# Optimization experiments

Hardware: AMD Instinct MI355X
Metric: run time of the kernel (lower is better)

Reference implementation:

```python
import jax, jax.numpy as jnp
import numpy as np

N, E, D_IN, D_H, D_OUT = 100000, 1600000, 128, 128, 16


def setup_inputs() -> dict:
    key = jax.random.key(0)
    k_x, k_e, k_w1, k_w2 = jax.random.split(key, 4)
    x = jax.random.normal(k_x, (N, D_IN), dtype=jnp.float32)
    edge_index = jax.random.randint(k_e, (2, E), 0, N, dtype=jnp.int64)
    # glorot-ish init for the two GCNConv weight matrices
    W1 = jax.random.normal(k_w1, (D_IN, D_H), dtype=jnp.float32) * (1.0 / np.sqrt(D_IN))
    b1 = jnp.zeros((D_H,), dtype=jnp.float32)
    W2 = jax.random.normal(k_w2, (D_H, D_OUT), dtype=jnp.float32) * (1.0 / np.sqrt(D_H))
    b2 = jnp.zeros((D_OUT,), dtype=jnp.float32)
    return {"x": x, "edge_index": edge_index, "W1": W1, "b1": b1, "W2": W2, "b2": b2}


def _gcn_conv(x, src, dst, norm, W, b, n):
    # linear transform, gather from source nodes, normalize, scatter-add to targets
    h = x @ W                                   # [N, d_out]
    msg = h[src] * norm[:, None]                # [E+N, d_out]
    return jax.ops.segment_sum(msg, dst, num_segments=n) + b


def reference(x, edge_index, W1, b1, W2, b2):
    n = x.shape[0]
    # GCNConv default: add self-loops, symmetric normalization D^-1/2 A D^-1/2
    loops = jnp.arange(n, dtype=edge_index.dtype)
    src = jnp.concatenate([edge_index[0], loops])
    dst = jnp.concatenate([edge_index[1], loops])
    deg = jax.ops.segment_sum(jnp.ones_like(dst, dtype=x.dtype), dst, num_segments=n)
    dinv = jnp.where(deg > 0, jax.lax.rsqrt(deg), 0.0)
    norm = dinv[src] * dinv[dst]                # [E+N]

    h = _gcn_conv(x, src, dst, norm, W1, b1, n)
    h = jax.nn.relu(h)
    # dropout is identity in eval mode (reference uses eval / deterministic path)
    out = _gcn_conv(h, src, dst, norm, W2, b2, n)
    return out
```

## Files before the change

kernel.cpp:

```cpp
#include <hip/hip_runtime.h>

typedef unsigned int uint;
typedef __attribute__((ext_vector_type(8))) short bf16x8;
typedef __attribute__((ext_vector_type(4))) float f32x4;

#define D_IN 128
#define D_H  128
#define D_OUT 16
#define NPC 512
#define NPCSH 9
#define CLDS 224
#define P1 256
#define XL_STRIDE 68
#define WT_STRIDE 68

static __device__ __forceinline__ float bflo(uint u) { return __uint_as_float(u << 16); }
static __device__ __forceinline__ float bfhi(uint u) { return __uint_as_float(u & 0xFFFF0000u); }
static __device__ __forceinline__ uint f2bf(float f) {
    uint b = __float_as_uint(f);
    return (b + 0x7FFFu + ((b >> 16) & 1u)) >> 16;
}
static __device__ __forceinline__ uint pk(float a, float b) {
    return f2bf(a) | (f2bf(b) << 16);
}


__global__ __launch_bounds__(256) void k_p1hist(const int* __restrict__ dst, int E, int N, int C,
                                                int chunk, int* __restrict__ hist1) {
    __shared__ int h[CLDS];
    int t = threadIdx.x, b = blockIdx.x;
    for (int i = t; i < C; i += 256) h[i] = 0;
    __syncthreads();
    int e0 = b * chunk, e1 = min(e0 + chunk, E);
    for (int e = e0 + t; e < e1; e += 256) {
        int d = dst[e];
        d = max(0, min(d, N - 1));
        atomicAdd(&h[d >> NPCSH], 1);
    }
    __syncthreads();
    int* hg = hist1 + (size_t)b * C;
    for (int i = t; i < C; i += 256) hg[i] = h[i];
}

__global__ __launch_bounds__(1024) void k_p1scan(int* __restrict__ hist1, int C,
                                                 int* __restrict__ cbase) {
    __shared__ int col[CLDS];
    __shared__ int sdata[1024];
    int t = threadIdx.x;
    for (int i = t; i < C; i += 1024) {
        int sum = 0;
        for (int b = 0; b < P1; b++) sum += hist1[(size_t)b * C + i];
        col[i] = sum;
    }
    __syncthreads();
    int v = (t < C) ? col[t] : 0;
    sdata[t] = v;
    __syncthreads();
    for (int off = 1; off < 1024; off <<= 1) {
        int x = (t >= off) ? sdata[t - off] : 0;
        __syncthreads();
        sdata[t] += x;
        __syncthreads();
    }
    int pos = sdata[t] - v;
    if (t < C) cbase[t] = pos;
    if (t == 1023) cbase[C] = sdata[1023];
    if (t < C) {
        int run = pos;
        for (int b = 0; b < P1; b++) {
            size_t idx = (size_t)b * C + t;
            int c = hist1[idx];
            hist1[idx] = run;
            run += c;
        }
    }
}

__global__ __launch_bounds__(256) void k_p1fill(const int* __restrict__ src,
                                                const int* __restrict__ dst, int E, int N, int C,
                                                int chunk, const int* __restrict__ hist1,
                                                uint* __restrict__ binned1) {
    __shared__ int cur[CLDS];
    int t = threadIdx.x, b = blockIdx.x;
    const int* hg = hist1 + (size_t)b * C;
    for (int i = t; i < C; i += 256) cur[i] = hg[i];
    __syncthreads();
    int e0 = b * chunk, e1 = min(e0 + chunk, E);
    for (int e = e0 + t; e < e1; e += 256) {
        int d = dst[e];
        d = max(0, min(d, N - 1));
        int s = src[e];
        s = max(0, min(s, N - 1));
        int p = atomicAdd(&cur[d >> NPCSH], 1);
        binned1[p] = ((uint)(d & (NPC - 1)) << 17) | (uint)s;
    }
}

__global__ __launch_bounds__(256) void k_p2(const uint* __restrict__ binned1,
                                            const int* __restrict__ cbase, int N,
                                            int* __restrict__ ssrc, int* __restrict__ rowptr,
                                            int* __restrict__ deg, float* __restrict__ dinv) {
    __shared__ int ncnt[NPC], nbase_[NPC];
    __shared__ int sdata[256];
    int c = blockIdx.x, t = threadIdx.x;
    int start = cbase[c], end = cbase[c + 1];
    for (int i = t; i < NPC; i += 256) ncnt[i] = 0;
    __syncthreads();
    for (int j = start + t; j < end; j += 256) atomicAdd(&ncnt[binned1[j] >> 17], 1);
    __syncthreads();
    int v0 = ncnt[2 * t], v1 = ncnt[2 * t + 1];
    int s = v0 + v1;
    sdata[t] = s;
    __syncthreads();
    for (int off = 1; off < 256; off <<= 1) {
        int xv = (t >= off) ? sdata[t - off] : 0;
        __syncthreads();
        sdata[t] += xv;
        __syncthreads();
    }
    int pre = sdata[t] - s;
    nbase_[2 * t] = start + pre;
    nbase_[2 * t + 1] = start + pre + v0;
    __syncthreads();
    for (int i = t; i < NPC; i += 256) {
        int node = c * NPC + i;
        if (node < N) {
            deg[node] = ncnt[i];
            rowptr[node] = nbase_[i];
            dinv[node] = rsqrtf((float)ncnt[i] + 1.0f);
        }
    }
    __syncthreads();
    for (int i = t; i < NPC; i += 256) ncnt[i] = nbase_[i];
    __syncthreads();
    for (int j = start + t; j < end; j += 256) {
        uint pe = binned1[j];
        int p = atomicAdd(&ncnt[pe >> 17], 1);
        ssrc[p] = (int)(pe & 0x1FFFFu);
    }
}


__global__ __launch_bounds__(256) void k_gemm1(const float* __restrict__ x,
                                               const float* __restrict__ W1,
                                               const float* __restrict__ dinv, int N,
                                               uint* __restrict__ hs_b) {
    __shared__ uint Wt[128 * WT_STRIDE];
    __shared__ uint xl[64 * XL_STRIDE];
    int t = threadIdx.x;
    int row0 = blockIdx.x * 64;
    for (int p = t; p < 64 * 128; p += 256) {
        int k2 = p >> 7, f = p & 127;
        float w0 = W1[(size_t)(2 * k2) * 128 + f];
        float w1 = W1[(size_t)(2 * k2 + 1) * 128 + f];
        Wt[f * WT_STRIDE + k2] = pk(w0, w1);
    }
    const float2* x2 = (const float2*)x;
    for (int p = t; p < 64 * 64; p += 256) {
        int r = p >> 6, c = p & 63;
        int gr = row0 + r;
        float2 v = (gr < N) ? x2[(size_t)gr * 64 + c] : make_float2(0.f, 0.f);
        xl[r * XL_STRIDE + c] = pk(v.x, v.y);
    }
    __syncthreads();
    int w = t >> 6, lane = t & 63;
    int q = lane >> 4, m = lane & 15;
    bf16x8 afr[4][4];
#pragma unroll
    for (int rt = 0; rt < 4; rt++)
#pragma unroll
        for (int kc = 0; kc < 4; kc++)
            afr[rt][kc] = *(const bf16x8*)&xl[(rt * 16 + m) * XL_STRIDE + kc * 16 + q * 4];
    f32x4 acc[2][4];
#pragma unroll
    for (int c = 0; c < 2; c++)
#pragma unroll
        for (int rt = 0; rt < 4; rt++) acc[c][rt] = (f32x4){0.f, 0.f, 0.f, 0.f};
#pragma unroll
    for (int c = 0; c < 2; c++) {
        int f = w * 32 + c * 16 + m;
#pragma unroll
        for (int kc = 0; kc < 4; kc++) {
            bf16x8 bfr = *(const bf16x8*)&Wt[f * WT_STRIDE + kc * 16 + q * 4];
#pragma unroll
            for (int rt = 0; rt < 4; rt++)
                acc[c][rt] =
                    __builtin_amdgcn_mfma_f32_16x16x32_bf16(afr[rt][kc], bfr, acc[c][rt], 0, 0, 0);
        }
    }
    __syncthreads();
    uint* outl = xl;
#pragma unroll
    for (int rt = 0; rt < 4; rt++) {
        int gb = row0 + rt * 16 + q * 4;
        float4 dv;
        if (gb + 3 < N) {
            dv = *(const float4*)&dinv[gb];
        } else {
            dv.x = (gb < N) ? dinv[gb] : 0.f;
            dv.y = (gb + 1 < N) ? dinv[gb + 1] : 0.f;
            dv.z = (gb + 2 < N) ? dinv[gb + 2] : 0.f;
            dv.w = (gb + 3 < N) ? dinv[gb + 3] : 0.f;
        }
        float dr[4] = {dv.x, dv.y, dv.z, dv.w};
#pragma unroll
        for (int c = 0; c < 2; c++) {
            f32x4 a = acc[c][rt];
#pragma unroll
            for (int r = 0; r < 4; r++) {
                float v = a[r] * dr[r];
                float vn = __shfl_xor(v, 1);
                if (!(lane & 1)) {
                    int row = rt * 16 + q * 4 + r;
                    int cp = (w * 32 + c * 16 + m) >> 1;
                    outl[row * 65 + cp] = pk(v, vn);
                }
            }
        }
    }
    __syncthreads();
    for (int p = t; p < 64 * 64; p += 256) {
        int r = p >> 6, cc = p & 63;
        int gr = row0 + r;
        if (gr < N) hs_b[(size_t)gr * 64 + cc] = outl[r * 65 + cc];
    }
}


__global__ __launch_bounds__(256) void k_agg1(const uint* __restrict__ hs_b,
                                              const int* __restrict__ rowptr,
                                              const int* __restrict__ deg,
                                              const int* __restrict__ ssrc,
                                              const float* __restrict__ dinv,
                                              const float2* __restrict__ b1, int N,
                                              uint* __restrict__ rh_b) {
    int w = threadIdx.x >> 6, lane = threadIdx.x & 63;
    int d = blockIdx.x * 4 + w;
    if (d >= N) return;
    int start = rowptr[d], cnt = deg[d];
    uint sv = hs_b[(size_t)d * 64 + lane];
    float a0 = bflo(sv), a1 = bfhi(sv);
    int base = 0;
    while (base < cnt) {
        int nb = min(cnt - base, 64);
        int idxv = (lane < nb) ? ssrc[start + base + lane] : 0;
        int j = 0;
        for (; j + 16 <= nb; j += 16) {
            uint u[16];
#pragma unroll
            for (int q = 0; q < 16; q++) {
                int i = __shfl(idxv, j + q);
                u[q] = hs_b[(size_t)i * 64 + lane];
            }
#pragma unroll
            for (int q = 0; q < 16; q++) {
                a0 += bflo(u[q]);
                a1 += bfhi(u[q]);
            }
        }
        for (; j + 4 <= nb; j += 4) {
            uint u[4];
#pragma unroll
            for (int q = 0; q < 4; q++) {
                int i = __shfl(idxv, j + q);
                u[q] = hs_b[(size_t)i * 64 + lane];
            }
#pragma unroll
            for (int q = 0; q < 4; q++) {
                a0 += bflo(u[q]);
                a1 += bfhi(u[q]);
            }
        }
        for (; j < nb; j++) {
            int i = __shfl(idxv, j);
            uint u = hs_b[(size_t)i * 64 + lane];
            a0 += bflo(u);
            a1 += bfhi(u);
        }
        base += nb;
    }
    float sc = dinv[d];
    float2 bb = b1[lane];
    rh_b[(size_t)d * 64 + lane] =
        pk(fmaxf(fmaf(a0, sc, bb.x), 0.f), fmaxf(fmaf(a1, sc, bb.y), 0.f));
}


__global__ __launch_bounds__(256) void k_gemm2(const uint* __restrict__ rh_b,
                                               const float* __restrict__ W2,
                                               const float* __restrict__ dinv, int N,
                                               uint* __restrict__ h2_b) {
    __shared__ float Wl[D_H * D_OUT];
    int t = threadIdx.x;
    for (int i = t; i < D_H * D_OUT; i += 256) Wl[i] = W2[i];
    __syncthreads();
    int r = blockIdx.x * 256 + t;
    if (r >= N) return;
    const uint* xrow = rh_b + (size_t)r * 64;
    float acc[16];
#pragma unroll
    for (int f = 0; f < 16; f++) acc[f] = 0.f;
    for (int c = 0; c < 16; c++) {
        uint4 xv = *(const uint4*)(xrow + c * 4);
        uint xs[4] = {xv.x, xv.y, xv.z, xv.w};
#pragma unroll
        for (int u = 0; u < 4; u++) {
            int k = c * 8 + u * 2;
            float x0 = bflo(xs[u]), x1 = bfhi(xs[u]);
            const float* w0 = &Wl[k * 16];
            const float* w1 = &Wl[(k + 1) * 16];
#pragma unroll
            for (int f = 0; f < 16; f++) acc[f] = fmaf(x0, w0[f], acc[f]);
#pragma unroll
            for (int f = 0; f < 16; f++) acc[f] = fmaf(x1, w1[f], acc[f]);
        }
    }
    float sc = dinv[r];
    uint o[8];
#pragma unroll
    for (int q = 0; q < 8; q++) o[q] = pk(acc[2 * q] * sc, acc[2 * q + 1] * sc);
    *(uint4*)&h2_b[(size_t)r * 8] = make_uint4(o[0], o[1], o[2], o[3]);
    *(uint4*)&h2_b[(size_t)r * 8 + 4] = make_uint4(o[4], o[5], o[6], o[7]);
}


__global__ __launch_bounds__(256) void k_agg2(const uint* __restrict__ h2_b,
                                              const int* __restrict__ rowptr,
                                              const int* __restrict__ deg,
                                              const int* __restrict__ ssrc,
                                              const float* __restrict__ dinv,
                                              const float* __restrict__ b2, int N,
                                              float2* __restrict__ out) {
    int w = threadIdx.x >> 6, lane = threadIdx.x & 63;
    int d = blockIdx.x * 4 + w;
    if (d >= N) return;
    int slot = lane >> 3, jp = lane & 7;
    int start = rowptr[d], cnt = deg[d];
    float a0 = 0.f, a1 = 0.f;
    if (slot == 0) {
        uint sv = h2_b[(size_t)d * 8 + jp];
        a0 = bflo(sv);
        a1 = bfhi(sv);
    }
    int base = 0;
    while (base < cnt) {
        int nb = min(cnt - base, 64);
        int idxv = (lane < nb) ? ssrc[start + base + lane] : 0;
        int ngroups = (nb + 7) >> 3;
        for (int g = 0; g < ngroups; g++) {
            int j = g * 8 + slot;
            int i = __shfl(idxv, j);
            if (j < nb) {
                uint hv = h2_b[(size_t)i * 8 + jp];
                a0 += bflo(hv);
                a1 += bfhi(hv);
            }
        }
        base += nb;
    }
    a0 += __shfl_xor(a0, 8);
    a1 += __shfl_xor(a1, 8);
    a0 += __shfl_xor(a0, 16);
    a1 += __shfl_xor(a1, 16);
    a0 += __shfl_xor(a0, 32);
    a1 += __shfl_xor(a1, 32);
    if (slot == 0) {
        float di = dinv[d];
        out[(size_t)d * 8 + jp] =
            make_float2(fmaf(a0, di, b2[2 * jp]), fmaf(a1, di, b2[2 * jp + 1]));
    }
}


extern "C" void kernel_launch(void* const* d_in, const int* in_sizes, int n_in,
                              void* d_out, int out_size, void* d_ws, size_t ws_size,
                              hipStream_t stream) {
    const float* x  = (const float*)d_in[0];
    const int*   ei = (const int*)d_in[1];
    const float* W1 = (const float*)d_in[2];
    const float* b1 = (const float*)d_in[3];
    const float* W2 = (const float*)d_in[4];
    const float* b2 = (const float*)d_in[5];
    int N = in_sizes[0] / D_IN;
    int E = in_sizes[1] / 2;
    const int* src = ei;
    const int* dst = ei + E;
    int C = (N + NPC - 1) / NPC;
    int chunk = (E + P1 - 1) / P1;

    char* ws = (char*)d_ws;
    size_t off = 0;
    auto alloc = [&](size_t bytes) -> char* {
        char* p = ws + off;
        off = (off + bytes + 255) & ~(size_t)255;
        return p;
    };
    int*   hist1   = (int*)alloc((size_t)P1 * C * 4);
    int*   cbase   = (int*)alloc((size_t)(C + 1) * 4);
    uint*  binned1 = (uint*)alloc((size_t)E * 4);
    int*   ssrc    = (int*)alloc((size_t)E * 4);
    int*   rowptr  = (int*)alloc((size_t)N * 4);
    int*   deg     = (int*)alloc((size_t)N * 4);
    float* dinv    = (float*)alloc((size_t)N * 4);
    uint*  hs_b    = (uint*)alloc((size_t)N * 64 * 4);
    uint*  rh_b    = (uint*)alloc((size_t)N * 64 * 4);
    uint*  h2_b    = hs_b;

    k_p1hist<<<P1, 256, 0, stream>>>(dst, E, N, C, chunk, hist1);
    k_p1scan<<<1, 1024, 0, stream>>>(hist1, C, cbase);
    k_p1fill<<<P1, 256, 0, stream>>>(src, dst, E, N, C, chunk, hist1, binned1);
    k_p2<<<C, 256, 0, stream>>>(binned1, cbase, N, ssrc, rowptr, deg, dinv);
    k_gemm1<<<(N + 63) / 64, 256, 0, stream>>>(x, W1, dinv, N, hs_b);
    k_agg1<<<(N + 3) / 4, 256, 0, stream>>>(hs_b, rowptr, deg, ssrc, dinv,
                                            (const float2*)b1, N, rh_b);
    k_gemm2<<<(N + 255) / 256, 256, 0, stream>>>(rh_b, W2, dinv, N, h2_b);
    k_agg2<<<(N + 3) / 4, 256, 0, stream>>>(h2_b, rowptr, deg, ssrc, dinv, b2, N,
                                            (float2*)d_out);
}
```

Measured before the change: 320.4 us.

## Transpose histogram layout for parallel scan; persistent gemm1 with prepacked W1

Stores the per-block bucket histogram transposed (bucket-major), so the single-block scan kernel can process each bucket with one wavefront doing a vectorized int4 load and shuffle prefix scan. This replaces the old serial 256-iteration per-thread loops. W1 is now packed to bf16 once by a new small kernel, and gemm1 becomes a persistent grid-stride kernel capped at 768 blocks. Each block loads the packed weights into LDS once and reuses them across many 64-row tiles, reading x with float4 loads. The cost is an extra launch, and the fill and hist kernels now do strided hist accesses.

```diff
diff --git a/kernel.cpp b/kernel.cpp
--- a/kernel.cpp
+++ b/kernel.cpp
@@ -38,8 +38,7 @@
         atomicAdd(&h[d >> NPCSH], 1);
     }
     __syncthreads();
-    int* hg = hist1 + (size_t)b * C;
-    for (int i = t; i < C; i += 256) hg[i] = h[i];
+    for (int i = t; i < C; i += 256) hist1[(size_t)i * P1 + b] = h[i];
 }
 
 __global__ __launch_bounds__(1024) void k_p1scan(int* __restrict__ hist1, int C,
@@ -47,10 +46,23 @@
     __shared__ int col[CLDS];
     __shared__ int sdata[1024];
     int t = threadIdx.x;
-    for (int i = t; i < C; i += 1024) {
-        int sum = 0;
-        for (int b = 0; b < P1; b++) sum += hist1[(size_t)b * C + i];
-        col[i] = sum;
+    int w = t >> 6, lane = t & 63;
+    for (int i = w; i < C; i += 16) {
+        int4 v = ((const int4*)hist1)[i * 64 + lane];
+        int s = v.x + v.y + v.z + v.w;
+        int inc = s;
+        for (int off = 1; off < 64; off <<= 1) {
+            int o = __shfl_up(inc, off);
+            if (lane >= off) inc += o;
+        }
+        int excl = inc - s;
+        int4 p;
+        p.x = excl;
+        p.y = excl + v.x;
+        p.z = excl + v.x + v.y;
+        p.w = excl + v.x + v.y + v.z;
+        ((int4*)hist1)[i * 64 + lane] = p;
+        if (lane == 63) col[i] = inc;
     }
     __syncthreads();
     int v = (t < C) ? col[t] : 0;
@@ -65,14 +77,13 @@
     int pos = sdata[t] - v;
     if (t < C) cbase[t] = pos;
     if (t == 1023) cbase[C] = sdata[1023];
-    if (t < C) {
-        int run = pos;
-        for (int b = 0; b < P1; b++) {
-            size_t idx = (size_t)b * C + t;
-            int c = hist1[idx];
-            hist1[idx] = run;
-            run += c;
-        }
+    if (t < C) col[t] = pos;
+    __syncthreads();
+    for (int i = w; i < C; i += 16) {
+        int base = col[i];
+        int4 p = ((int4*)hist1)[i * 64 + lane];
+        p.x += base; p.y += base; p.z += base; p.w += base;
+        ((int4*)hist1)[i * 64 + lane] = p;
     }
 }
 
@@ -82,8 +93,7 @@
                                                 uint* __restrict__ binned1) {
     __shared__ int cur[CLDS];
     int t = threadIdx.x, b = blockIdx.x;
-    const int* hg = hist1 + (size_t)b * C;
-    for (int i = t; i < C; i += 256) cur[i] = hg[i];
+    for (int i = t; i < C; i += 256) cur[i] = hist1[(size_t)i * P1 + b];
     __syncthreads();
     int e0 = b * chunk, e1 = min(e0 + chunk, E);
     for (int e = e0 + t; e < e1; e += 256) {
@@ -141,88 +151,100 @@
 }
 
 
-__global__ __launch_bounds__(256) void k_gemm1(const float* __restrict__ x,
-                                               const float* __restrict__ W1,
+__global__ __launch_bounds__(256) void k_packW1(const float* __restrict__ W1,
+                                                uint* __restrict__ W1p) {
+    int t = blockIdx.x * 256 + threadIdx.x;
+    if (t >= 64 * 128) return;
+    int k2 = t >> 7, f = t & 127;
+    float w0 = W1[(size_t)(2 * k2) * 128 + f];
+    float w1 = W1[(size_t)(2 * k2 + 1) * 128 + f];
+    W1p[t] = pk(w0, w1);
+}
+
+
+__global__ __launch_bounds__(256) void k_gemm1(const uint* __restrict__ W1p,
+                                               const float* __restrict__ x,
                                                const float* __restrict__ dinv, int N,
-                                               uint* __restrict__ hs_b) {
+                                               uint* __restrict__ hs_b, int ntiles) {
     __shared__ uint Wt[128 * WT_STRIDE];
     __shared__ uint xl[64 * XL_STRIDE];
     int t = threadIdx.x;
-    int row0 = blockIdx.x * 64;
     for (int p = t; p < 64 * 128; p += 256) {
         int k2 = p >> 7, f = p & 127;
-        float w0 = W1[(size_t)(2 * k2) * 128 + f];
-        float w1 = W1[(size_t)(2 * k2 + 1) * 128 + f];
-        Wt[f * WT_STRIDE + k2] = pk(w0, w1);
-    }
-    const float2* x2 = (const float2*)x;
-    for (int p = t; p < 64 * 64; p += 256) {
-        int r = p >> 6, c = p & 63;
-        int gr = row0 + r;
-        float2 v = (gr < N) ? x2[(size_t)gr * 64 + c] : make_float2(0.f, 0.f);
-        xl[r * XL_STRIDE + c] = pk(v.x, v.y);
-    }
-    __syncthreads();
+        Wt[f * WT_STRIDE + k2] = W1p[p];
+    }
     int w = t >> 6, lane = t & 63;
     int q = lane >> 4, m = lane & 15;
-    bf16x8 afr[4][4];
-#pragma unroll
-    for (int rt = 0; rt < 4; rt++)
-#pragma unroll
-        for (int kc = 0; kc < 4; kc++)
-            afr[rt][kc] = *(const bf16x8*)&xl[(rt * 16 + m) * XL_STRIDE + kc * 16 + q * 4];
-    f32x4 acc[2][4];
-#pragma unroll
-    for (int c = 0; c < 2; c++)
-#pragma unroll
-        for (int rt = 0; rt < 4; rt++) acc[c][rt] = (f32x4){0.f, 0.f, 0.f, 0.f};
-#pragma unroll
-    for (int c = 0; c < 2; c++) {
-        int f = w * 32 + c * 16 + m;
-#pragma unroll
-        for (int kc = 0; kc < 4; kc++) {
-            bf16x8 bfr = *(const bf16x8*)&Wt[f * WT_STRIDE + kc * 16 + q * 4];
-#pragma unroll
-            for (int rt = 0; rt < 4; rt++)
-                acc[c][rt] =
-                    __builtin_amdgcn_mfma_f32_16x16x32_bf16(afr[rt][kc], bfr, acc[c][rt], 0, 0, 0);
-        }
-    }
-    __syncthreads();
-    uint* outl = xl;
-#pragma unroll
-    for (int rt = 0; rt < 4; rt++) {
-        int gb = row0 + rt * 16 + q * 4;
-        float4 dv;
-        if (gb + 3 < N) {
-            dv = *(const float4*)&dinv[gb];
-        } else {
-            dv.x = (gb < N) ? dinv[gb] : 0.f;
-            dv.y = (gb + 1 < N) ? dinv[gb + 1] : 0.f;
-            dv.z = (gb + 2 < N) ? dinv[gb + 2] : 0.f;
-            dv.w = (gb + 3 < N) ? dinv[gb + 3] : 0.f;
-        }
-        float dr[4] = {dv.x, dv.y, dv.z, dv.w};
+    const float4* x4 = (const float4*)x;
+    for (int tile = blockIdx.x; tile < ntiles; tile += gridDim.x) {
+        int row0 = tile * 64;
+        __syncthreads();
+        for (int p = t; p < 64 * 32; p += 256) {
+            int r = p >> 5, c2 = p & 31;
+            int gr = row0 + r;
+            float4 v = (gr < N) ? x4[(size_t)gr * 32 + c2] : make_float4(0.f, 0.f, 0.f, 0.f);
+            *(uint2*)&xl[r * XL_STRIDE + 2 * c2] = make_uint2(pk(v.x, v.y), pk(v.z, v.w));
+        }
+        __syncthreads();
+        bf16x8 afr[4][4];
+#pragma unroll
+        for (int rt = 0; rt < 4; rt++)
+#pragma unroll
+            for (int kc = 0; kc < 4; kc++)
+                afr[rt][kc] = *(const bf16x8*)&xl[(rt * 16 + m) * XL_STRIDE + kc * 16 + q * 4];
+        f32x4 acc[2][4];
+#pragma unroll
+        for (int c = 0; c < 2; c++)
+#pragma unroll
+            for (int rt = 0; rt < 4; rt++) acc[c][rt] = (f32x4){0.f, 0.f, 0.f, 0.f};
 #pragma unroll
         for (int c = 0; c < 2; c++) {
-            f32x4 a = acc[c][rt];
-#pragma unroll
-            for (int r = 0; r < 4; r++) {
-                float v = a[r] * dr[r];
-                float vn = __shfl_xor(v, 1);
-                if (!(lane & 1)) {
-                    int row = rt * 16 + q * 4 + r;
-                    int cp = (w * 32 + c * 16 + m) >> 1;
-                    outl[row * 65 + cp] = pk(v, vn);
+            int f = w * 32 + c * 16 + m;
+#pragma unroll
+            for (int kc = 0; kc < 4; kc++) {
+                bf16x8 bfr = *(const bf16x8*)&Wt[f * WT_STRIDE + kc * 16 + q * 4];
+#pragma unroll
+                for (int rt = 0; rt < 4; rt++)
+                    acc[c][rt] = __builtin_amdgcn_mfma_f32_16x16x32_bf16(afr[rt][kc], bfr,
+                                                                         acc[c][rt], 0, 0, 0);
+            }
+        }
+        __syncthreads();
+        uint* outl = xl;
+#pragma unroll
+        for (int rt = 0; rt < 4; rt++) {
+            int gb = row0 + rt * 16 + q * 4;
+            float4 dv;
+            if (gb + 3 < N) {
+                dv = *(const float4*)&dinv[gb];
+            } else {
+                dv.x = (gb < N) ? dinv[gb] : 0.f;
+                dv.y = (gb + 1 < N) ? dinv[gb + 1] : 0.f;
+                dv.z = (gb + 2 < N) ? dinv[gb + 2] : 0.f;
+                dv.w = (gb + 3 < N) ? dinv[gb + 3] : 0.f;
+            }
+            float dr[4] = {dv.x, dv.y, dv.z, dv.w};
+#pragma unroll
+            for (int c = 0; c < 2; c++) {
+                f32x4 a = acc[c][rt];
+#pragma unroll
+                for (int r = 0; r < 4; r++) {
+                    float v = a[r] * dr[r];
+                    float vn = __shfl_xor(v, 1);
+                    if (!(lane & 1)) {
+                        int row = rt * 16 + q * 4 + r;
+                        int cp = (w * 32 + c * 16 + m) >> 1;
+                        outl[row * 65 + cp] = pk(v, vn);
+                    }
                 }
             }
         }
-    }
-    __syncthreads();
-    for (int p = t; p < 64 * 64; p += 256) {
-        int r = p >> 6, cc = p & 63;
-        int gr = row0 + r;
-        if (gr < N) hs_b[(size_t)gr * 64 + cc] = outl[r * 65 + cc];
+        __syncthreads();
+        for (int p = t; p < 64 * 64; p += 256) {
+            int r = p >> 6, cc = p & 63;
+            int gr = row0 + r;
+            if (gr < N) hs_b[(size_t)gr * 64 + cc] = outl[r * 65 + cc];
+        }
     }
 }
 
@@ -387,6 +409,7 @@
     const int* dst = ei + E;
     int C = (N + NPC - 1) / NPC;
     int chunk = (E + P1 - 1) / P1;
+    int ntiles = (N + 63) / 64;
 
     char* ws = (char*)d_ws;
     size_t off = 0;
@@ -402,15 +425,18 @@
     int*   rowptr  = (int*)alloc((size_t)N * 4);
     int*   deg     = (int*)alloc((size_t)N * 4);
     float* dinv    = (float*)alloc((size_t)N * 4);
+    uint*  W1p     = (uint*)alloc((size_t)64 * 128 * 4);
     uint*  hs_b    = (uint*)alloc((size_t)N * 64 * 4);
     uint*  rh_b    = (uint*)alloc((size_t)N * 64 * 4);
     uint*  h2_b    = hs_b;
 
+    k_packW1<<<32, 256, 0, stream>>>(W1, W1p);
     k_p1hist<<<P1, 256, 0, stream>>>(dst, E, N, C, chunk, hist1);
     k_p1scan<<<1, 1024, 0, stream>>>(hist1, C, cbase);
     k_p1fill<<<P1, 256, 0, stream>>>(src, dst, E, N, C, chunk, hist1, binned1);
     k_p2<<<C, 256, 0, stream>>>(binned1, cbase, N, ssrc, rowptr, deg, dinv);
-    k_gemm1<<<(N + 63) / 64, 256, 0, stream>>>(x, W1, dinv, N, hs_b);
+    int g1 = min(768, ntiles);
+    k_gemm1<<<g1, 256, 0, stream>>>(W1p, x, dinv, N, hs_b, ntiles);
     k_agg1<<<(N + 3) / 4, 256, 0, stream>>>(hs_b, rowptr, deg, ssrc, dinv,
                                             (const float2*)b1, N, rh_b);
     k_gemm2<<<(N + 255) / 256, 256, 0, stream>>>(rh_b, W2, dinv, N, h2_b);
```

After: 295.1 us. 7.9% less time.
